# Kernel tuning notes

Hardware: AMD Instinct MI355X
Metric: run time of the kernel (lower is better)

## Reference

```python
import jax, jax.numpy as jnp
import numpy as np

SIG_LEVEL = 2
UNIT = 128
SEQ = 64
BATCH = 256
SIG_DIM = UNIT + UNIT ** 2  # truncated signature dim for level 2
LN_EPS = 1e-5


def _signature(path, level):
    """Truncated path signature up to `level` via Chen's relation.
    path: (B, T, d) -> (B, d + d^2 + ... + d^level).
    Each segment contributes exp(dx): level-m term dx^{outer m}/m!.
    """
    B, T, d = path.shape
    dx = path[:, 1:] - path[:, :-1]  # (B, T-1, d)
    init = [jnp.zeros((B, d ** k), dtype=path.dtype) for k in range(1, level + 1)]

    def step(S, dxt):  # S: list of (B, d^k); dxt: (B, d)
        # P[m] = dxt^{outer m} / m!, flattened (B, d^m)
        P = [jnp.ones((B, 1), dtype=dxt.dtype), dxt]
        for m in range(2, level + 1):
            P.append((P[-1][:, :, None] * dxt[:, None, :]).reshape(B, d ** m) / m)
        newS = []
        for k in range(1, level + 1):
            s = P[k]  # j = 0 term (S_0 = 1)
            for j in range(1, k + 1):
                s = s + (S[j - 1][:, :, None] * P[k - j][:, None, :]).reshape(B, d ** k)
            newS.append(s)
        return newS, None

    S, _ = jax.lax.scan(step, init, jnp.swapaxes(dx, 0, 1))
    return jnp.concatenate(S, axis=-1)


def _grn_softmax(sig, W2, b2, W1, b1, Wg, bg, Wv, bv, Ws, bs, gamma, beta):
    # TFT-style gated residual network with softmax output activation.
    h = jax.nn.elu(sig @ W2 + b2)          # (B, unit)
    h = h @ W1 + b1                        # (B, unit)
    glu = jax.nn.sigmoid(h @ Wg + bg) * (h @ Wv + bv)
    skip = sig @ Ws + bs                   # residual projection sig_dim -> unit
    y = skip + glu
    mu = jnp.mean(y, axis=-1, keepdims=True)
    var = jnp.var(y, axis=-1, keepdims=True)
    y = (y - mu) * jax.lax.rsqrt(var + LN_EPS) * gamma + beta
    return jax.nn.softmax(y, axis=-1)


def setup_inputs() -> dict:
    key = jax.random.key(0)
    ks = jax.random.split(key, 16)
    s = 0.02
    return {
        "inputs": jax.random.normal(ks[0], (BATCH, SEQ, UNIT), dtype=jnp.float32),
        "time_kernel": jnp.ones((SEQ, 1), dtype=jnp.float32),
        "Wd": jax.random.normal(ks[1], (UNIT, UNIT), dtype=jnp.float32) * s,
        "bd": jnp.zeros((UNIT,), dtype=jnp.float32),
        "W2": jax.random.normal(ks[2], (SIG_DIM, UNIT), dtype=jnp.float32) * s,
        "b2": jnp.zeros((UNIT,), dtype=jnp.float32),
        "W1": jax.random.normal(ks[3], (UNIT, UNIT), dtype=jnp.float32) * s,
        "b1": jnp.zeros((UNIT,), dtype=jnp.float32),
        "Wg": jax.random.normal(ks[4], (UNIT, UNIT), dtype=jnp.float32) * s,
        "bg": jnp.zeros((UNIT,), dtype=jnp.float32),
        "Wv": jax.random.normal(ks[5], (UNIT, UNIT), dtype=jnp.float32) * s,
        "bv": jnp.zeros((UNIT,), dtype=jnp.float32),
        "Ws": jax.random.normal(ks[6], (SIG_DIM, UNIT), dtype=jnp.float32) * s,
        "bs": jnp.zeros((UNIT,), dtype=jnp.float32),
        "gamma": jnp.ones((UNIT,), dtype=jnp.float32),
        "beta": jnp.zeros((UNIT,), dtype=jnp.float32),
    }


def reference(inputs, time_kernel, Wd, bd, W2, b2, W1, b1, Wg, bg, Wv, bv, Ws, bs, gamma, beta):
    x = time_kernel * inputs                         # (B, T, d) time weighting
    sig = _signature(x, SIG_LEVEL)                   # (B, sig_dim)
    weights = _grn_softmax(sig, W2, b2, W1, b1, Wg, bg, Wv, bv, Ws, bs, gamma, beta)  # (B, d)
    dense_out = x @ Wd + bd                          # (B, T, d); dropout is identity at eval
    return dense_out * weights[:, None, :]
```

## Files before the change

### kernel.cpp

```cpp
#include <hip/hip_runtime.h>
#include <math.h>

#define SD 16512
#define NCH 129
#define CHUNK 65536
#define LN_EPS 1e-5f

typedef __attribute__((ext_vector_type(4))) float f32x4;
typedef __attribute__((ext_vector_type(8))) short bf16x8;

__device__ __forceinline__ unsigned bfpack(float lo, float hi) {
    unsigned a = __builtin_bit_cast(unsigned, lo);
    unsigned b = __builtin_bit_cast(unsigned, hi);
    a = (a + 0x7FFFu + ((a >> 16) & 1u)) >> 16;
    b = (b + 0x7FFFu + ((b >> 16) & 1u)) >> 16;
    return a | (b << 16);
}
__device__ __forceinline__ unsigned short bf1(float x) {
    unsigned a = __builtin_bit_cast(unsigned, x);
    return (unsigned short)((a + 0x7FFFu + ((a >> 16) & 1u)) >> 16);
}

__global__ __launch_bounds__(256) void k_sig(const float* __restrict__ x,
                                             const float* __restrict__ tk,
                                             const float* __restrict__ Wd,
                                             unsigned short* __restrict__ sig,
                                             unsigned short* __restrict__ xbf,
                                             unsigned short* __restrict__ WdTg) {
    __shared__ unsigned short Ut[128][72];
    __shared__ unsigned short DXt[128][72];
    __shared__ float tks[64];
    int tid = threadIdx.x;
    int b = blockIdx.x;

    if (b == 256) {
        int d = tid & 127, kh = tid >> 7;
        unsigned* dst = (unsigned*)WdTg;
        for (int kk = 0; kk < 64; kk += 2) {
            int k = kh * 64 + kk;
            float v0 = Wd[(size_t)k * 128 + d];
            float v1 = Wd[(size_t)(k + 1) * 128 + d];
            dst[d * 64 + ((kh * 64 + kk) >> 1)] = bfpack(v0, v1);
        }
        return;
    }

    if (tid < 64) tks[tid] = tk[tid];
    __syncthreads();

    const float* xb = x + (size_t)b * 8192;
    unsigned short* xbb = xbf + (size_t)b * 8192;
    int i = tid & 127, th = tid >> 7;

    float x0 = tks[0] * xb[i];
    float xa = tks[th * 32] * xb[(size_t)(th * 32) * 128 + i];
    for (int tp = 0; tp < 16; ++tp) {
        int p = th * 16 + tp;
        int t0 = 2 * p;
        float xv = tks[t0 + 1] * xb[(size_t)(t0 + 1) * 128 + i];
        float dx0 = xv - xa, u0 = 0.5f * (xa + xv) - x0;
        float dx1, u1, xc;
        if (p == 31) { dx1 = 0.f; u1 = 0.f; xc = 0.f; }
        else {
            xc = tks[t0 + 2] * xb[(size_t)(t0 + 2) * 128 + i];
            dx1 = xc - xv; u1 = 0.5f * (xv + xc) - x0;
        }
        *(unsigned*)&Ut[i][t0]  = bfpack(u0, u1);
        *(unsigned*)&DXt[i][t0] = bfpack(dx0, dx1);
        xbb[(size_t)t0 * 128 + i]       = bf1(xa);
        xbb[(size_t)(t0 + 1) * 128 + i] = bf1(xv);
        if (p == 31) sig[(size_t)b * SD + i] = bf1(xv - x0);
        xa = xc;
    }
    __syncthreads();

    int w = tid >> 6, lane = tid & 63;
    int wm = w >> 1, wn = w & 1;
    int l15 = lane & 15, lg = lane >> 4;
    f32x4 acc[4][4];
    #pragma unroll
    for (int m = 0; m < 4; ++m)
        #pragma unroll
        for (int n = 0; n < 4; ++n) acc[m][n] = (f32x4){0.f, 0.f, 0.f, 0.f};

    #pragma unroll
    for (int ks = 0; ks < 2; ++ks) {
        bf16x8 af[4], bfv[4];
        #pragma unroll
        for (int m = 0; m < 4; ++m)
            af[m] = *(const bf16x8*)&Ut[wm * 64 + m * 16 + l15][ks * 32 + lg * 8];
        #pragma unroll
        for (int n = 0; n < 4; ++n)
            bfv[n] = *(const bf16x8*)&DXt[wn * 64 + n * 16 + l15][ks * 32 + lg * 8];
        #pragma unroll
        for (int m = 0; m < 4; ++m)
            #pragma unroll
            for (int n = 0; n < 4; ++n)
                acc[m][n] = __builtin_amdgcn_mfma_f32_16x16x32_bf16(af[m], bfv[n], acc[m][n], 0, 0, 0);
    }

    unsigned short* sp = sig + (size_t)b * SD + 128;
    #pragma unroll
    for (int m = 0; m < 4; ++m)
        #pragma unroll
        for (int n = 0; n < 4; ++n)
            #pragma unroll
            for (int rr = 0; rr < 4; ++rr)
                sp[(size_t)(wm * 64 + m * 16 + lg * 4 + rr) * 128 + wn * 64 + n * 16 + l15]
                    = bf1(acc[m][n][rr]);
}

__global__ __launch_bounds__(512, 2) void k_gemm(const unsigned short* __restrict__ sig,
                                                 const float* __restrict__ W2,
                                                 const float* __restrict__ Ws,
                                                 float* __restrict__ partial) {
    __shared__ unsigned short As[256 * 128];
    __shared__ unsigned short Bs[64 * 128];

    int p = blockIdx.x;
    int xc = p & 7, o = p >> 3;
    int lid = (xc < 4 ? xc * 65 : 260 + (xc - 4) * 64) + o;
    int ch = lid >> 2, nt = lid & 3;
    const float* W = (nt < 2) ? W2 : Ws;
    int ntc = (nt & 1) * 64;
    int kb = ch * 128;

    int tid = threadIdx.x;

    {
        int row = tid >> 1, half = tid & 1;
        const unsigned short* src = sig + (size_t)row * SD + kb + half * 64;
        int sw = (row & 7) << 3;
        #pragma unroll
        for (int j = 0; j < 8; ++j) {
            uint4 v = *(const uint4*)(src + j * 8);
            int cu = (half * 64 + j * 8) ^ sw;
            *(uint4*)&As[row * 128 + cu] = v;
        }
    }
    {
        int k = tid >> 2, cq = (tid & 3) * 16;
        const float* wp = W + (size_t)(kb + k) * 128 + ntc + cq;
        float v[16];
        #pragma unroll
        for (int u = 0; u < 4; ++u) {
            f32x4 t = *(const f32x4*)(wp + u * 4);
            v[u * 4] = t[0]; v[u * 4 + 1] = t[1]; v[u * 4 + 2] = t[2]; v[u * 4 + 3] = t[3];
        }
        #pragma unroll
        for (int u = 0; u < 16; ++u) {
            int c = cq + u;
            Bs[c * 128 + (k ^ ((c & 7) << 3))] = bf1(v[u]);
        }
    }
    __syncthreads();

    int w = tid >> 6, lane = tid & 63;
    int l15 = lane & 15, lg = lane >> 4;
    int rbase = w * 32;

    f32x4 acc[2][4];
    #pragma unroll
    for (int m = 0; m < 2; ++m)
        #pragma unroll
        for (int n = 0; n < 4; ++n) acc[m][n] = (f32x4){0.f, 0.f, 0.f, 0.f};

    #pragma unroll
    for (int ks = 0; ks < 4; ++ks) {
        bf16x8 af[2], bfv[4];
        #pragma unroll
        for (int m = 0; m < 2; ++m) {
            int row = rbase + m * 16 + l15;
            af[m] = *(const bf16x8*)&As[row * 128 + ((ks * 32 + lg * 8) ^ ((row & 7) << 3))];
        }
        #pragma unroll
        for (int n = 0; n < 4; ++n) {
            int col = n * 16 + l15;
            bfv[n] = *(const bf16x8*)&Bs[col * 128 + ((ks * 32 + lg * 8) ^ ((col & 7) << 3))];
        }
        #pragma unroll
        for (int m = 0; m < 2; ++m)
            #pragma unroll
            for (int n = 0; n < 4; ++n)
                acc[m][n] = __builtin_amdgcn_mfma_f32_16x16x32_bf16(af[m], bfv[n], acc[m][n], 0, 0, 0);
    }

    float* Pp = partial + (size_t)ch * CHUNK + nt * 64;
    #pragma unroll
    for (int m = 0; m < 2; ++m)
        #pragma unroll
        for (int n = 0; n < 4; ++n)
            #pragma unroll
            for (int rr = 0; rr < 4; ++rr)
                Pp[(size_t)(rbase + m * 16 + lg * 4 + rr) * 256 + n * 16 + l15]
                    = acc[m][n][rr];
}

__global__ __launch_bounds__(512) void k_tail(const float* __restrict__ partial,
                                              const unsigned short* __restrict__ xbf,
                                              const unsigned short* __restrict__ WdTg,
                                              const float* __restrict__ b2,
                                              const float* __restrict__ W1,
                                              const float* __restrict__ b1,
                                              const float* __restrict__ Wg,
                                              const float* __restrict__ bg,
                                              const float* __restrict__ Wv,
                                              const float* __restrict__ bv,
                                              const float* __restrict__ bs,
                                              const float* __restrict__ gamma,
                                              const float* __restrict__ beta,
                                              const float* __restrict__ bd,
                                              float* __restrict__ out) {
    __shared__ float hs[128], ss[128], h2s[128];
    __shared__ float red4[4][128], rtmp[2][256];
    __shared__ float ys[128], es[128], wts[128];

    int b = blockIdx.x, tid = threadIdx.x;
    int lane = tid & 63;
    int l15 = lane & 15, lg = lane >> 4;

    {
        int c = tid & 255, h = tid >> 8;
        float s = 0.f;
        const float* Pp = partial + (size_t)b * 256 + c;
        #pragma unroll 8
        for (int ch = h; ch < NCH; ch += 2) s += Pp[(size_t)ch * CHUNK];
        rtmp[h][c] = s;
    }
    __syncthreads();
    if (tid < 256) {
        float rsum = rtmp[0][tid] + rtmp[1][tid];
        if (tid < 128) {
            float hp = rsum + b2[tid];
            hs[tid] = hp > 0.f ? hp : expm1f(hp);
        } else {
            ss[tid - 128] = rsum + bs[tid - 128];
        }
    }
    __syncthreads();

    int c = tid & 127;
    {
        int qt = tid >> 7;
        float s = 0.f;
        int kbq = qt * 32;
        #pragma unroll 8
        for (int k = 0; k < 32; ++k) s += hs[kbq + k] * W1[(size_t)(kbq + k) * 128 + c];
        red4[qt][c] = s;
    }
    __syncthreads();
    if (tid < 128)
        h2s[tid] = red4[0][tid] + red4[1][tid] + red4[2][tid] + red4[3][tid] + b1[tid];
    __syncthreads();
    {
        int idx = tid >> 7, sel = idx & 1, kh = idx >> 1;
        const float* Wx = sel ? Wv : Wg;
        float s = 0.f;
        int kbq = kh * 64;
        #pragma unroll 8
        for (int k = 0; k < 64; ++k) s += h2s[kbq + k] * Wx[(size_t)(kbq + k) * 128 + c];
        red4[idx][c] = s;
    }
    __syncthreads();
    if (tid < 128) {
        float g = 1.f / (1.f + expf(-(red4[0][c] + red4[2][c] + bg[c])));
        float v = red4[1][c] + red4[3][c] + bv[c];
        ys[c] = ss[c] + g * v;
    }
    __syncthreads();
    if (tid < 128) {
        float sum = 0.f, sq = 0.f;
        for (int k = 0; k < 128; ++k) { float v = ys[k]; sum += v; sq += v * v; }
        float mu = sum * (1.f / 128.f);
        float var = sq * (1.f / 128.f) - mu * mu;
        float rs = rsqrtf(var + LN_EPS);
        es[c] = (ys[c] - mu) * rs * gamma[c] + beta[c];
    }
    __syncthreads();
    if (tid < 128) {
        float m = -1e30f;
        for (int k = 0; k < 128; ++k) m = fmaxf(m, es[k]);
        ys[c] = expf(es[c] - m);
    }
    __syncthreads();
    if (tid < 128) {
        float se = 0.f;
        for (int k = 0; k < 128; ++k) se += ys[k];
        wts[c] = ys[c] / se;
    }
    __syncthreads();

    int w4 = tid >> 6;
    const unsigned short* xrow = xbf + (size_t)b * 8192;
    f32x4 dacc[4];
    #pragma unroll
    for (int fm = 0; fm < 4; ++fm) dacc[fm] = (f32x4){0.f, 0.f, 0.f, 0.f};
    #pragma unroll
    for (int ks = 0; ks < 4; ++ks) {
        bf16x8 av[4], bv2;
        #pragma unroll
        for (int fm = 0; fm < 4; ++fm)
            av[fm] = *(const bf16x8*)(xrow + (size_t)(fm * 16 + l15) * 128 + ks * 32 + lg * 8);
        bv2 = *(const bf16x8*)(WdTg + (size_t)(w4 * 16 + l15) * 128 + ks * 32 + lg * 8);
        #pragma unroll
        for (int fm = 0; fm < 4; ++fm)
            dacc[fm] = __builtin_amdgcn_mfma_f32_16x16x32_bf16(av[fm], bv2, dacc[fm], 0, 0, 0);
    }
    int dcol = w4 * 16 + l15;
    float bdv = bd[dcol], wtv = wts[dcol];
    #pragma unroll
    for (int fm = 0; fm < 4; ++fm)
        #pragma unroll
        for (int rr = 0; rr < 4; ++rr) {
            int t = fm * 16 + lg * 4 + rr;
            out[(size_t)b * 8192 + (size_t)t * 128 + dcol] = (dacc[fm][rr] + bdv) * wtv;
        }
}

extern "C" void kernel_launch(void* const* d_in, const int* in_sizes, int n_in,
                              void* d_out, int out_size, void* d_ws, size_t ws_size,
                              hipStream_t stream) {
    const float* inputs = (const float*)d_in[0];
    const float* tk     = (const float*)d_in[1];
    const float* Wd     = (const float*)d_in[2];
    const float* bd     = (const float*)d_in[3];
    const float* W2     = (const float*)d_in[4];
    const float* b2     = (const float*)d_in[5];
    const float* W1     = (const float*)d_in[6];
    const float* b1     = (const float*)d_in[7];
    const float* Wg     = (const float*)d_in[8];
    const float* bg     = (const float*)d_in[9];
    const float* Wv     = (const float*)d_in[10];
    const float* bv     = (const float*)d_in[11];
    const float* Wsk    = (const float*)d_in[12];
    const float* bs     = (const float*)d_in[13];
    const float* gamma  = (const float*)d_in[14];
    const float* beta   = (const float*)d_in[15];
    float* out = (float*)d_out;

    char* ws = (char*)d_ws;
    unsigned short* sig  = (unsigned short*)ws;
    float* partial       = (float*)(ws + 8454144);
    unsigned short* xbf  = (unsigned short*)(ws + 42270720);
    unsigned short* WdTg = (unsigned short*)(ws + 46465024);

    k_sig <<<257, 256, 0, stream>>>(inputs, tk, Wd, sig, xbf, WdTg);
    k_gemm<<<516, 512, 0, stream>>>(sig, W2, Wsk, partial);
    k_tail<<<256, 512, 0, stream>>>(partial, xbf, WdTg, b2, W1, b1, Wg, bg, Wv, bv,
                                    bs, gamma, beta, bd, out);
}
```

Measured before the change: 47.69 us.

## Store split-K partials as packed bf16 and widen signature kernel to 512 threads

The split-K GEMM now writes its per-chunk partial sums as bf16 pairs packed two batch rows per 32-bit word, which halves the partial buffer, and the tail kernel unpacks and sums them in fp32. The signature kernel moves to 512 threads per block: each thread handles half as many time steps and each wave computes a 64x32 MFMA tile instead of 64x64. The goal is to cut global memory traffic for the 129-way reduction and to raise parallelism in the first kernel. The cost is rounding every partial to bf16 before the sum, which adds error that compounds across the 129 chunks.

```diff
diff --git a/kernel.cpp b/kernel.cpp
--- a/kernel.cpp
+++ b/kernel.cpp
@@ -3,7 +3,7 @@
 
 #define SD 16512
 #define NCH 129
-#define CHUNK 65536
+#define CHUNKP 32768
 #define LN_EPS 1e-5f
 
 typedef __attribute__((ext_vector_type(4))) float f32x4;
@@ -21,7 +21,7 @@
     return (unsigned short)((a + 0x7FFFu + ((a >> 16) & 1u)) >> 16);
 }
 
-__global__ __launch_bounds__(256) void k_sig(const float* __restrict__ x,
+__global__ __launch_bounds__(512) void k_sig(const float* __restrict__ x,
                                              const float* __restrict__ tk,
                                              const float* __restrict__ Wd,
                                              unsigned short* __restrict__ sig,
@@ -36,11 +36,11 @@
     if (b == 256) {
         int d = tid & 127, kh = tid >> 7;
         unsigned* dst = (unsigned*)WdTg;
-        for (int kk = 0; kk < 64; kk += 2) {
-            int k = kh * 64 + kk;
+        for (int kk = 0; kk < 32; kk += 2) {
+            int k = kh * 32 + kk;
             float v0 = Wd[(size_t)k * 128 + d];
             float v1 = Wd[(size_t)(k + 1) * 128 + d];
-            dst[d * 64 + ((kh * 64 + kk) >> 1)] = bfpack(v0, v1);
+            dst[d * 64 + (k >> 1)] = bfpack(v0, v1);
         }
         return;
     }
@@ -53,9 +53,10 @@
     int i = tid & 127, th = tid >> 7;
 
     float x0 = tks[0] * xb[i];
-    float xa = tks[th * 32] * xb[(size_t)(th * 32) * 128 + i];
-    for (int tp = 0; tp < 16; ++tp) {
-        int p = th * 16 + tp;
+    float xa = tks[th * 16] * xb[(size_t)(th * 16) * 128 + i];
+    #pragma unroll
+    for (int tp = 0; tp < 8; ++tp) {
+        int p = th * 8 + tp;
         int t0 = 2 * p;
         float xv = tks[t0 + 1] * xb[(size_t)(t0 + 1) * 128 + i];
         float dx0 = xv - xa, u0 = 0.5f * (xa + xv) - x0;
@@ -75,27 +76,27 @@
     __syncthreads();
 
     int w = tid >> 6, lane = tid & 63;
-    int wm = w >> 1, wn = w & 1;
+    int wm = w >> 2, wn = w & 3;
     int l15 = lane & 15, lg = lane >> 4;
-    f32x4 acc[4][4];
+    f32x4 acc[4][2];
     #pragma unroll
     for (int m = 0; m < 4; ++m)
         #pragma unroll
-        for (int n = 0; n < 4; ++n) acc[m][n] = (f32x4){0.f, 0.f, 0.f, 0.f};
+        for (int n = 0; n < 2; ++n) acc[m][n] = (f32x4){0.f, 0.f, 0.f, 0.f};
 
     #pragma unroll
     for (int ks = 0; ks < 2; ++ks) {
-        bf16x8 af[4], bfv[4];
+        bf16x8 af[4], bfv[2];
         #pragma unroll
         for (int m = 0; m < 4; ++m)
             af[m] = *(const bf16x8*)&Ut[wm * 64 + m * 16 + l15][ks * 32 + lg * 8];
         #pragma unroll
-        for (int n = 0; n < 4; ++n)
-            bfv[n] = *(const bf16x8*)&DXt[wn * 64 + n * 16 + l15][ks * 32 + lg * 8];
+        for (int n = 0; n < 2; ++n)
+            bfv[n] = *(const bf16x8*)&DXt[wn * 32 + n * 16 + l15][ks * 32 + lg * 8];
         #pragma unroll
         for (int m = 0; m < 4; ++m)
             #pragma unroll
-            for (int n = 0; n < 4; ++n)
+            for (int n = 0; n < 2; ++n)
                 acc[m][n] = __builtin_amdgcn_mfma_f32_16x16x32_bf16(af[m], bfv[n], acc[m][n], 0, 0, 0);
     }
 
@@ -103,17 +104,17 @@
     #pragma unroll
     for (int m = 0; m < 4; ++m)
         #pragma unroll
-        for (int n = 0; n < 4; ++n)
+        for (int n = 0; n < 2; ++n)
             #pragma unroll
             for (int rr = 0; rr < 4; ++rr)
-                sp[(size_t)(wm * 64 + m * 16 + lg * 4 + rr) * 128 + wn * 64 + n * 16 + l15]
+                sp[(size_t)(wm * 64 + m * 16 + lg * 4 + rr) * 128 + wn * 32 + n * 16 + l15]
                     = bf1(acc[m][n][rr]);
 }
 
 __global__ __launch_bounds__(512, 2) void k_gemm(const unsigned short* __restrict__ sig,
                                                  const float* __restrict__ W2,
                                                  const float* __restrict__ Ws,
-                                                 float* __restrict__ partial) {
+                                                 unsigned* __restrict__ partial_p) {
     __shared__ unsigned short As[256 * 128];
     __shared__ unsigned short Bs[64 * 128];
 
@@ -185,18 +186,19 @@
                 acc[m][n] = __builtin_amdgcn_mfma_f32_16x16x32_bf16(af[m], bfv[n], acc[m][n], 0, 0, 0);
     }
 
-    float* Pp = partial + (size_t)ch * CHUNK + nt * 64;
+    unsigned* Pp = partial_p + (size_t)ch * CHUNKP + nt * 64;
     #pragma unroll
     for (int m = 0; m < 2; ++m)
         #pragma unroll
-        for (int n = 0; n < 4; ++n)
-            #pragma unroll
-            for (int rr = 0; rr < 4; ++rr)
-                Pp[(size_t)(rbase + m * 16 + lg * 4 + rr) * 256 + n * 16 + l15]
-                    = acc[m][n][rr];
-}
-
-__global__ __launch_bounds__(512) void k_tail(const float* __restrict__ partial,
+        for (int n = 0; n < 4; ++n) {
+            int r0 = rbase + m * 16 + lg * 4;
+            int cc = n * 16 + l15;
+            Pp[(size_t)(r0 >> 1) * 256 + cc]       = bfpack(acc[m][n][0], acc[m][n][1]);
+            Pp[(size_t)((r0 >> 1) + 1) * 256 + cc] = bfpack(acc[m][n][2], acc[m][n][3]);
+        }
+}
+
+__global__ __launch_bounds__(512) void k_tail(const unsigned* __restrict__ partial_p,
                                               const unsigned short* __restrict__ xbf,
                                               const unsigned short* __restrict__ WdTg,
                                               const float* __restrict__ b2,
@@ -222,9 +224,14 @@
     {
         int c = tid & 255, h = tid >> 8;
         float s = 0.f;
-        const float* Pp = partial + (size_t)b * 256 + c;
+        const unsigned* Pp = partial_p + (size_t)(b >> 1) * 256 + c;
+        bool hi = (b & 1) != 0;
         #pragma unroll 8
-        for (int ch = h; ch < NCH; ch += 2) s += Pp[(size_t)ch * CHUNK];
+        for (int ch = h; ch < NCH; ch += 2) {
+            unsigned u = Pp[(size_t)ch * CHUNKP];
+            unsigned hw = hi ? (u & 0xffff0000u) : (u << 16);
+            s += __builtin_bit_cast(float, hw);
+        }
         rtmp[h][c] = s;
     }
     __syncthreads();
@@ -340,12 +347,12 @@
 
     char* ws = (char*)d_ws;
     unsigned short* sig  = (unsigned short*)ws;
-    float* partial       = (float*)(ws + 8454144);
-    unsigned short* xbf  = (unsigned short*)(ws + 42270720);
-    unsigned short* WdTg = (unsigned short*)(ws + 46465024);
-
-    k_sig <<<257, 256, 0, stream>>>(inputs, tk, Wd, sig, xbf, WdTg);
-    k_gemm<<<516, 512, 0, stream>>>(sig, W2, Wsk, partial);
-    k_tail<<<256, 512, 0, stream>>>(partial, xbf, WdTg, b2, W1, b1, Wg, bg, Wv, bv,
+    unsigned* partial_p  = (unsigned*)(ws + 8454144);
+    unsigned short* xbf  = (unsigned short*)(ws + 25362432);
+    unsigned short* WdTg = (unsigned short*)(ws + 29556736);
+
+    k_sig <<<257, 512, 0, stream>>>(inputs, tk, Wd, sig, xbf, WdTg);
+    k_gemm<<<516, 512, 0, stream>>>(sig, W2, Wsk, partial_p);
+    k_tail<<<256, 512, 0, stream>>>(partial_p, xbf, WdTg, b2, W1, b1, Wg, bg, Wv, bv,
                                     bs, gamma, beta, bd, out);
 }
```

Result: faster. 44.58 us (-6.5%).
